# Optimization experiments

Hardware: AMD Instinct MI355X
Metric: run time of the kernel (lower is better)

## Reference

```python
import jax, jax.numpy as jnp
import numpy as np

B1, B2, CHUNK, HID, T = 64, 16, 128, 64, 131072
N_CHUNKS = 128


def setup_inputs() -> dict:
    key = jax.random.key(0)
    ks = jax.random.split(key, 12)
    # positive prices so log(p) is finite
    p = jax.random.uniform(ks[0], (T, 2), jnp.float32) * 2.0 + 0.5
    inds = jax.random.randint(ks[1], (B1,), 0, 100000, dtype=jnp.int32)
    open_slices = jax.random.randint(ks[2], (B1, B2, 1), 0, T, dtype=jnp.int32)
    ls_probs = jax.random.uniform(ks[3], (B1, B2, 1, 1), jnp.float32)
    open_probs = jax.random.uniform(ks[4], (B1, B2, 1, 1), jnp.float32)
    open_hx = jax.random.normal(ks[5], (B1, B2, 2, HID), jnp.float32) * 0.1
    s = 1.0 / np.sqrt(HID)
    # torch nn.LSTM params: gate order i,f,g,o
    W_ih = jax.random.uniform(ks[6], (4 * HID, 2), jnp.float32, -s, s)
    W_hh = jax.random.uniform(ks[7], (4 * HID, HID), jnp.float32, -s, s)
    b_ih = jax.random.uniform(ks[8], (4 * HID,), jnp.float32, -s, s)
    b_hh = jax.random.uniform(ks[9], (4 * HID,), jnp.float32, -s, s)
    W_out = jax.random.uniform(ks[10], (1, HID), jnp.float32, -s, s)
    b_out = jax.random.uniform(ks[11], (1,), jnp.float32, -s, s)
    return {"inds": inds, "p": p, "ls_probs": ls_probs, "open_probs": open_probs,
            "open_slices": open_slices, "open_hx": open_hx,
            "W_ih": W_ih, "W_hh": W_hh, "b_ih": b_ih, "b_hh": b_hh,
            "W_out": W_out, "b_out": b_out, "n_chunks": N_CHUNKS}


def reference(inds, p, ls_probs, open_probs, open_slices, open_hx,
              W_ih, W_hh, b_ih, b_hh, W_out, b_out, n_chunks):
    b1, b2 = open_hx.shape[:2]
    hid = open_hx.shape[-1]
    C = CHUNK
    h0 = open_hx[:, :, 0, :].reshape(b1 * b2, hid)
    c0 = open_hx[:, :, 1, :].reshape(b1 * b2, hid)
    open_logp = jnp.log(p[open_slices])  # (b1, b2, 1, 2)
    # sliding-window gather base: idx[i,j,t] = inds[i] + j + t (per-chunk offset added in scan)
    base = (inds[:, None, None]
            + jnp.arange(b2, dtype=inds.dtype)[None, :, None]
            + jnp.arange(C, dtype=inds.dtype)[None, None, :])  # (b1, b2, C)
    bias = b_ih + b_hh

    def lstm_chunk(x, h, c):  # x: (N, C, 2)
        xg = x @ W_ih.T + bias  # precompute input projection: (N, C, 4H)
        def step(carry, xg_t):
            h, c = carry
            g = xg_t + h @ W_hh.T
            i, f, gg, o = jnp.split(g, 4, axis=-1)
            c = jax.nn.sigmoid(f) * c + jax.nn.sigmoid(i) * jnp.tanh(gg)
            h = jax.nn.sigmoid(o) * jnp.tanh(c)
            return (h, c), h
        (h, c), hs = jax.lax.scan(step, (h, c), xg.swapaxes(0, 1))
        return hs.swapaxes(0, 1), h, c  # (N, C, H)

    def chunk_step(carry, offset):
        h, c, last_nd, loss = carry
        idx = base + offset * C                      # (b1, b2, C)
        p_chunk = p[idx]                             # (b1, b2, C, 2)
        x = p_chunk - p_chunk[:, :, :1, :]           # re-center on first step of chunk
        out, h, c = lstm_chunk(x.reshape(b1 * b2, C, 2), h, c)
        probs = jax.nn.sigmoid(out.reshape(b1, b2, C, hid) @ W_out.T + b_out)  # (b1,b2,C,1)
        not_done = last_nd * jnp.cumprod(1.0 - probs[:, :, :-1], axis=2)       # (b1,b2,C-1,1)
        probs = jnp.concatenate([probs[:, :, :1], probs[:, :, 1:] * not_done], axis=2)
        last_nd = not_done[:, :, -1:, :]
        logp = jnp.log(p_chunk)
        payoff = ls_probs * (logp - open_logp) + (1.0 - ls_probs) * (open_logp - logp)
        loss = loss + jnp.sum(open_probs * probs * payoff)
        return (h, c, last_nd, loss), None

    init = (h0, c0, jnp.ones((b1, b2, 1, 1), p.dtype), jnp.zeros((), p.dtype))
    (_, _, _, loss), _ = jax.lax.scan(chunk_step, init, jnp.arange(n_chunks))
    return loss
```

## Files before the change

### kernel.cpp

```cpp
#include <hip/hip_runtime.h>


#define CH  128
#define HID 64

typedef __fp16 half8 __attribute__((ext_vector_type(8)));
typedef float  f32x4 __attribute__((ext_vector_type(4)));
typedef int    int4v __attribute__((ext_vector_type(4)));

__device__ __forceinline__ float rlf(float v, int l) {
  return __builtin_bit_cast(float, __builtin_amdgcn_readlane(__builtin_bit_cast(int, v), l));
}
__device__ __forceinline__ int packh(float a, float b) {
  return __builtin_bit_cast(int, __builtin_amdgcn_cvt_pkrtz(a, b));
}
__device__ __forceinline__ float frcp(float x) { return __builtin_amdgcn_rcpf(x); }
__device__ __forceinline__ float sigm(float x) { return frcp(1.0f + __expf(-x)); }
__device__ __forceinline__ float tanh_(float x) {
  float e = __expf(2.0f * x);
  return 1.0f - 2.0f * frcp(e + 1.0f);
}
template <int CTRL, int RMASK>
__device__ __forceinline__ float dpp_add(float v) {
  int x = __builtin_amdgcn_update_dpp(0, __builtin_bit_cast(int, v), CTRL, RMASK, 0xF, true);
  return v + __builtin_bit_cast(float, x);
}
__device__ __forceinline__ float dpp_xor1(float v) {
  int x = __builtin_amdgcn_update_dpp(0, __builtin_bit_cast(int, v), 0xB1, 0xF, 0xF, true);
  return __builtin_bit_cast(float, x);
}
__device__ __forceinline__ float dpp_wave_sum(float v) {
  v = dpp_add<0x111, 0xF>(v);
  v = dpp_add<0x112, 0xF>(v);
  v = dpp_add<0x114, 0xF>(v);
  v = dpp_add<0x118, 0xF>(v);
  v = dpp_add<0x142, 0xA>(v);
  v = dpp_add<0x143, 0xC>(v);
  return v;
}

__global__ __attribute__((amdgpu_flat_work_group_size(128, 128), amdgpu_waves_per_eu(2, 2)))
void pc_lstm_kernel(const int* __restrict__ inds,
                    const float* __restrict__ p,
                    const float* __restrict__ ls_probs,
                    const float* __restrict__ open_probs,
                    const int* __restrict__ open_slices,
                    const float* __restrict__ open_hx,
                    const float* __restrict__ W_ih,
                    const float* __restrict__ W_hh,
                    const float* __restrict__ b_ih,
                    const float* __restrict__ b_hh,
                    const float* __restrict__ W_out,
                    const float* __restrict__ b_out,
                    const int* __restrict__ n_chunks_p,
                    float* __restrict__ out)
{
  __shared__ __fp16 ring[2][CH][HID];
  __shared__ int prod;
  __shared__ int cons;

  const int tid  = threadIdx.x;
  const int wv   = tid >> 6;
  const int lane = tid & 63;
  const int s    = blockIdx.x;
  const int n_chunks = n_chunks_p[0];
  const int tbase = inds[s >> 4] + (s & 15);
  const float2* p2 = (const float2*)p;

  if (tid == 0) { prod = 0; cons = 0; }
  __syncthreads();

  if (wv == 0) {
    const int kg = lane >> 4;
    const int cc = lane & 15;

    half8 Wb[32];
#pragma unroll
    for (int t = 0; t < 16; ++t) {
#pragma unroll
      for (int kc = 0; kc < 2; ++kc) {
        const float* wp = W_hh + (16 * t + cc) * HID + 32 * kc + 8 * kg;
        half8 w;
#pragma unroll
        for (int j = 0; j < 8; ++j) w[j] = (__fp16)wp[j];
        Wb[2 * t + kc] = w;
      }
    }

    float wxa[4], wxb[4], bb[4];
#pragma unroll
    for (int g = 0; g < 4; ++g) {
      const int r = g * HID + lane;
      wxa[g] = W_ih[2 * r];
      wxb[g] = W_ih[2 * r + 1];
      bb[g]  = b_ih[r] + b_hh[r];
    }
    float h = open_hx[(s * 2 + 0) * HID + lane];
    float c = open_hx[(s * 2 + 1) * HID + lane];

    int ia0[4], ia1[4];
#pragma unroll
    for (int w = 0; w < 4; ++w) {
      ia0[w] = 4 * (8 * kg + 2 * w);
      ia1[w] = 4 * (32 + 8 * kg + 2 * w);
    }

    const bool u1 = (lane & 16) != 0;
    const bool u2 = (lane & 32) != 0;
    const f32x4 zero4 = {0.f, 0.f, 0.f, 0.f};

    float2 curA = p2[tbase + lane];
    float2 curB = p2[tbase + HID + lane];
    float2 nxtA = curA, nxtB = curB;

    for (int off = 0; off < n_chunks; ++off) {
      if (off) { curA = nxtA; curB = nxtB; }
      const float px0 = rlf(curA.x, 0);
      const float px1 = rlf(curA.y, 0);
      float2 xA, xB;
      xA.x = curA.x - px0; xA.y = curA.y - px1;
      xB.x = curB.x - px0; xB.y = curB.y - px1;
      if (off + 1 < n_chunks) {
        const int nb = tbase + (off + 1) * CH;
        nxtA = p2[nb + lane];
        nxtB = p2[nb + HID + lane];
      }
      while (__hip_atomic_load(&cons, __ATOMIC_ACQUIRE, __HIP_MEMORY_SCOPE_WORKGROUP) + 2 <= off)
        __builtin_amdgcn_s_sleep(8);

      __fp16* slot = &ring[off & 1][0][0];
#pragma unroll
      for (int hf = 0; hf < 2; ++hf) {
        const float xcx = hf ? xB.x : xA.x;
        const float xcy = hf ? xB.y : xA.y;
#pragma unroll 1
        for (int tl = 0; tl < 64; ++tl) {
          const int hp = packh(h, dpp_xor1(h));
          int4v A0, A1;
#pragma unroll
          for (int w = 0; w < 4; ++w) {
            A0[w] = __builtin_amdgcn_ds_bpermute(ia0[w], hp);
            A1[w] = __builtin_amdgcn_ds_bpermute(ia1[w], hp);
          }
          const half8 a0 = __builtin_bit_cast(half8, A0);
          const half8 a1 = __builtin_bit_cast(half8, A1);

          const float x0 = rlf(xcx, tl);
          const float x1 = rlf(xcy, tl);

          float pa[4];
#pragma unroll
          for (int g = 0; g < 4; ++g) {
            f32x4 q0 = __builtin_amdgcn_mfma_f32_16x16x32_f16(a0, Wb[8 * g + 0], zero4, 0, 0, 0);
            q0       = __builtin_amdgcn_mfma_f32_16x16x32_f16(a1, Wb[8 * g + 1], q0,    0, 0, 0);
            f32x4 q1 = __builtin_amdgcn_mfma_f32_16x16x32_f16(a0, Wb[8 * g + 2], zero4, 0, 0, 0);
            q1       = __builtin_amdgcn_mfma_f32_16x16x32_f16(a1, Wb[8 * g + 3], q1,    0, 0, 0);
            f32x4 q2 = __builtin_amdgcn_mfma_f32_16x16x32_f16(a0, Wb[8 * g + 4], zero4, 0, 0, 0);
            q2       = __builtin_amdgcn_mfma_f32_16x16x32_f16(a1, Wb[8 * g + 5], q2,    0, 0, 0);
            f32x4 q3 = __builtin_amdgcn_mfma_f32_16x16x32_f16(a0, Wb[8 * g + 6], zero4, 0, 0, 0);
            q3       = __builtin_amdgcn_mfma_f32_16x16x32_f16(a1, Wb[8 * g + 7], q3,    0, 0, 0);
            const float s01 = u1 ? q1[0] : q0[0];
            const float s23 = u1 ? q3[0] : q2[0];
            const float dg  = u2 ? s23 : s01;
            pa[g] = fmaf(x0, wxa[g], fmaf(x1, wxb[g], dg + bb[g]));
          }

          const float ig = sigm(pa[0]);
          const float fg = sigm(pa[1]);
          const float gg = tanh_(pa[2]);
          const float og = sigm(pa[3]);
          c = fmaf(fg, c, ig * gg);
          h = og * tanh_(c);

          const int tt = hf * 64 + tl;
          slot[tt * HID + lane] = (__fp16)h;
        }
      }
      if (lane == 0)
        __hip_atomic_store(&prod, off + 1, __ATOMIC_RELEASE, __HIP_MEMORY_SCOPE_WORKGROUP);
    }
  } else {
    const float wo   = W_out[lane];
    const float bout = b_out[0];
    const int   os   = open_slices[s];
    const float OL   = __logf(p[2 * os]) + __logf(p[2 * os + 1]);
    const float coef = open_probs[s] * (2.0f * ls_probs[s] - 1.0f);

    float S = 1.0f, D = 1.0f, lsum = 0.0f, psum = 0.0f;

    for (int off = 0; off < n_chunks; ++off) {
      const int cb = tbase + off * CH;
      const float2 cA = p2[cb + lane];
      const float2 cB = p2[cb + HID + lane];
      const float LA = __logf(cA.x) + __logf(cA.y);
      const float LB = __logf(cB.x) + __logf(cB.y);

      while (__hip_atomic_load(&prod, __ATOMIC_ACQUIRE, __HIP_MEMORY_SCOPE_WORKGROUP) <= off)
        __builtin_amdgcn_s_sleep(32);

      const __fp16* slot = &ring[off & 1][0][0];
#pragma unroll 1
      for (int tt = 0; tt < CH; ++tt) {
        const float hv = (float)slot[tt * HID + lane];
        const float z  = rlf(dpp_wave_sum(hv * wo), 63);
        const float pr = sigm(z + bout);
        const float Lt = (tt < 64) ? rlf(LA, tt) : rlf(LB, tt - 64);
        const float pn = (tt == 0) ? pr : pr * D;
        lsum = fmaf(pn, Lt, lsum);
        psum += pn;
        if (tt == 0)           D = S * (1.0f - pr);
        else if (tt < CH - 1)  D *= (1.0f - pr);
        else                   S = D;
      }
      if (lane == 0)
        __hip_atomic_store(&cons, off + 1, __ATOMIC_RELEASE, __HIP_MEMORY_SCOPE_WORKGROUP);
    }
    if (lane == 0) atomicAdd(out, coef * (lsum - OL * psum));
  }
}

extern "C" void kernel_launch(void* const* d_in, const int* in_sizes, int n_in,
                              void* d_out, int out_size, void* d_ws, size_t ws_size,
                              hipStream_t stream) {
  (void)hipMemsetAsync(d_out, 0, sizeof(float), stream);

  pc_lstm_kernel<<<dim3(1024), dim3(128), 0, stream>>>(
      (const int*)d_in[0],
      (const float*)d_in[1],
      (const float*)d_in[2],
      (const float*)d_in[3],
      (const int*)d_in[4],
      (const float*)d_in[5],
      (const float*)d_in[6],
      (const float*)d_in[7],
      (const float*)d_in[8],
      (const float*)d_in[9],
      (const float*)d_in[10],
      (const float*)d_in[11],
      (const int*)d_in[12],
      (float*)d_out);
}
```

Baseline: 7.032 ms.

## Pack four sequences per wave into the MFMA batch and shrink grid

Each block now processes four LSTM sequences instead of one. The 16 batch rows of the 16x16x32 MFMA carry 4 sequences × 4 hidden slices, so the MFMA work that was mostly wasted on a single sequence now serves four, and the grid shrinks from 1024 to 256 blocks. The producer wave also computes the W_out dot product itself through a row-level DPP reduction and passes only per-step logits through LDS, replacing the fp16 hidden-state ring. The cost is four times the gate math per lane per step, fewer blocks to fill the GPU, and a relaxed waves-per-EU hint.

```diff
diff --git a/kernel.cpp b/kernel.cpp
--- a/kernel.cpp
+++ b/kernel.cpp
@@ -8,8 +8,11 @@
 typedef float  f32x4 __attribute__((ext_vector_type(4)));
 typedef int    int4v __attribute__((ext_vector_type(4)));
 
-__device__ __forceinline__ float rlf(float v, int l) {
-  return __builtin_bit_cast(float, __builtin_amdgcn_readlane(__builtin_bit_cast(int, v), l));
+__device__ __forceinline__ int bperm(int byte_idx, int src) {
+  return __builtin_amdgcn_ds_bpermute(byte_idx, src);
+}
+__device__ __forceinline__ float bpermf(int byte_idx, float src) {
+  return __builtin_bit_cast(float, __builtin_amdgcn_ds_bpermute(byte_idx, __builtin_bit_cast(int, src)));
 }
 __device__ __forceinline__ int packh(float a, float b) {
   return __builtin_bit_cast(int, __builtin_amdgcn_cvt_pkrtz(a, b));
@@ -29,17 +32,21 @@
   int x = __builtin_amdgcn_update_dpp(0, __builtin_bit_cast(int, v), 0xB1, 0xF, 0xF, true);
   return __builtin_bit_cast(float, x);
 }
-__device__ __forceinline__ float dpp_wave_sum(float v) {
+__device__ __forceinline__ float dpp_row_sum(float v) {
   v = dpp_add<0x111, 0xF>(v);
   v = dpp_add<0x112, 0xF>(v);
   v = dpp_add<0x114, 0xF>(v);
   v = dpp_add<0x118, 0xF>(v);
+  return v;
+}
+__device__ __forceinline__ float dpp_wave_sum(float v) {
+  v = dpp_row_sum(v);
   v = dpp_add<0x142, 0xA>(v);
   v = dpp_add<0x143, 0xC>(v);
   return v;
 }
 
-__global__ __attribute__((amdgpu_flat_work_group_size(128, 128), amdgpu_waves_per_eu(2, 2)))
+__global__ __attribute__((amdgpu_flat_work_group_size(128, 128), amdgpu_waves_per_eu(1, 2)))
 void pc_lstm_kernel(const int* __restrict__ inds,
                     const float* __restrict__ p,
                     const float* __restrict__ ls_probs,
@@ -55,7 +62,7 @@
                     const int* __restrict__ n_chunks_p,
                     float* __restrict__ out)
 {
-  __shared__ __fp16 ring[2][CH][HID];
+  __shared__ float zring[2][CH][4];
   __shared__ int prod;
   __shared__ int cons;
 
@@ -64,15 +71,18 @@
   const int lane = tid & 63;
   const int s    = blockIdx.x;
   const int n_chunks = n_chunks_p[0];
-  const int tbase = inds[s >> 4] + (s & 15);
+  const int q    = lane >> 4;
+  const int cc   = lane & 15;
+  const int sq   = 4 * s + q;
+  const int tb   = inds[sq >> 4] + (sq & 15);
   const float2* p2 = (const float2*)p;
+  const int xbase = 4 * (16 * q);
 
   if (tid == 0) { prod = 0; cons = 0; }
   __syncthreads();
 
   if (wv == 0) {
     const int kg = lane >> 4;
-    const int cc = lane & 15;
 
     half8 Wb[32];
 #pragma unroll
@@ -87,135 +97,158 @@
       }
     }
 
-    float wxa[4], wxb[4], bb[4];
-#pragma unroll
-    for (int g = 0; g < 4; ++g) {
-      const int r = g * HID + lane;
-      wxa[g] = W_ih[2 * r];
-      wxb[g] = W_ih[2 * r + 1];
-      bb[g]  = b_ih[r] + b_hh[r];
-    }
-    float h = open_hx[(s * 2 + 0) * HID + lane];
-    float c = open_hx[(s * 2 + 1) * HID + lane];
-
-    int ia0[4], ia1[4];
-#pragma unroll
-    for (int w = 0; w < 4; ++w) {
-      ia0[w] = 4 * (8 * kg + 2 * w);
-      ia1[w] = 4 * (32 + 8 * kg + 2 * w);
-    }
-
-    const bool u1 = (lane & 16) != 0;
-    const bool u2 = (lane & 32) != 0;
+    float wxa[4][4], wxb[4][4], bb[4][4];
+#pragma unroll
+    for (int g = 0; g < 4; ++g)
+#pragma unroll
+      for (int u = 0; u < 4; ++u) {
+        const int r = g * HID + cc + 16 * u;
+        wxa[g][u] = W_ih[2 * r];
+        wxb[g][u] = W_ih[2 * r + 1];
+        bb[g][u]  = b_ih[r] + b_hh[r];
+      }
+    float wo[4];
+#pragma unroll
+    for (int u = 0; u < 4; ++u) wo[u] = W_out[cc + 16 * u];
+
+    float h[4], c[4];
+#pragma unroll
+    for (int u = 0; u < 4; ++u) {
+      h[u] = open_hx[(sq * 2 + 0) * HID + cc + 16 * u];
+      c[u] = open_hx[(sq * 2 + 1) * HID + cc + 16 * u];
+    }
+
+    const int qa = cc >> 2;
+    int idxA[4];
+#pragma unroll
+    for (int w = 0; w < 4; ++w)
+      idxA[w] = 4 * (16 * qa + ((8 * kg) & 15) + 2 * w);
+    const bool kgLow = (kg < 2);
     const f32x4 zero4 = {0.f, 0.f, 0.f, 0.f};
 
-    float2 curA = p2[tbase + lane];
-    float2 curB = p2[tbase + HID + lane];
-    float2 nxtA = curA, nxtB = curB;
-
     for (int off = 0; off < n_chunks; ++off) {
-      if (off) { curA = nxtA; curB = nxtB; }
-      const float px0 = rlf(curA.x, 0);
-      const float px1 = rlf(curA.y, 0);
-      float2 xA, xB;
-      xA.x = curA.x - px0; xA.y = curA.y - px1;
-      xB.x = curB.x - px0; xB.y = curB.y - px1;
-      if (off + 1 < n_chunks) {
-        const int nb = tbase + (off + 1) * CH;
-        nxtA = p2[nb + lane];
-        nxtB = p2[nb + HID + lane];
+      float xsx[8], xsy[8];
+      {
+        float2 tmp[8];
+        const long cb = (long)tb + (long)off * CH;
+#pragma unroll
+        for (int m = 0; m < 8; ++m) tmp[m] = p2[cb + cc + 16 * m];
+        const float px0 = bpermf(xbase, tmp[0].x);
+        const float px1 = bpermf(xbase, tmp[0].y);
+#pragma unroll
+        for (int m = 0; m < 8; ++m) {
+          xsx[m] = tmp[m].x - px0;
+          xsy[m] = tmp[m].y - px1;
+        }
       }
       while (__hip_atomic_load(&cons, __ATOMIC_ACQUIRE, __HIP_MEMORY_SCOPE_WORKGROUP) + 2 <= off)
         __builtin_amdgcn_s_sleep(8);
 
-      __fp16* slot = &ring[off & 1][0][0];
-#pragma unroll
-      for (int hf = 0; hf < 2; ++hf) {
-        const float xcx = hf ? xB.x : xA.x;
-        const float xcy = hf ? xB.y : xA.y;
+      float* zslot = &zring[off & 1][0][0];
+#pragma unroll
+      for (int m = 0; m < 8; ++m) {
 #pragma unroll 1
-        for (int tl = 0; tl < 64; ++tl) {
-          const int hp = packh(h, dpp_xor1(h));
+        for (int tt = 0; tt < 16; ++tt) {
+          const int t = 16 * m + tt;
+          const float hx0 = dpp_xor1(h[0]), hx1 = dpp_xor1(h[1]);
+          const float hx2 = dpp_xor1(h[2]), hx3 = dpp_xor1(h[3]);
+          const int hp0 = packh(h[0], hx0), hp1 = packh(h[1], hx1);
+          const int hp2 = packh(h[2], hx2), hp3 = packh(h[3], hx3);
+          const int hA = kgLow ? hp0 : hp1;
+          const int hB = kgLow ? hp2 : hp3;
           int4v A0, A1;
 #pragma unroll
           for (int w = 0; w < 4; ++w) {
-            A0[w] = __builtin_amdgcn_ds_bpermute(ia0[w], hp);
-            A1[w] = __builtin_amdgcn_ds_bpermute(ia1[w], hp);
+            A0[w] = bperm(idxA[w], hA);
+            A1[w] = bperm(idxA[w], hB);
           }
           const half8 a0 = __builtin_bit_cast(half8, A0);
           const half8 a1 = __builtin_bit_cast(half8, A1);
 
-          const float x0 = rlf(xcx, tl);
-          const float x1 = rlf(xcy, tl);
-
-          float pa[4];
-#pragma unroll
-          for (int g = 0; g < 4; ++g) {
-            f32x4 q0 = __builtin_amdgcn_mfma_f32_16x16x32_f16(a0, Wb[8 * g + 0], zero4, 0, 0, 0);
-            q0       = __builtin_amdgcn_mfma_f32_16x16x32_f16(a1, Wb[8 * g + 1], q0,    0, 0, 0);
-            f32x4 q1 = __builtin_amdgcn_mfma_f32_16x16x32_f16(a0, Wb[8 * g + 2], zero4, 0, 0, 0);
-            q1       = __builtin_amdgcn_mfma_f32_16x16x32_f16(a1, Wb[8 * g + 3], q1,    0, 0, 0);
-            f32x4 q2 = __builtin_amdgcn_mfma_f32_16x16x32_f16(a0, Wb[8 * g + 4], zero4, 0, 0, 0);
-            q2       = __builtin_amdgcn_mfma_f32_16x16x32_f16(a1, Wb[8 * g + 5], q2,    0, 0, 0);
-            f32x4 q3 = __builtin_amdgcn_mfma_f32_16x16x32_f16(a0, Wb[8 * g + 6], zero4, 0, 0, 0);
-            q3       = __builtin_amdgcn_mfma_f32_16x16x32_f16(a1, Wb[8 * g + 7], q3,    0, 0, 0);
-            const float s01 = u1 ? q1[0] : q0[0];
-            const float s23 = u1 ? q3[0] : q2[0];
-            const float dg  = u2 ? s23 : s01;
-            pa[g] = fmaf(x0, wxa[g], fmaf(x1, wxb[g], dg + bb[g]));
+          const int xi = xbase + 4 * tt;
+          const float x0 = bpermf(xi, xsx[m]);
+          const float x1 = bpermf(xi, xsy[m]);
+
+#pragma unroll
+          for (int u = 0; u < 4; ++u) {
+            f32x4 e0 = __builtin_amdgcn_mfma_f32_16x16x32_f16(a0, Wb[     2 * u], zero4, 0, 0, 0);
+            e0       = __builtin_amdgcn_mfma_f32_16x16x32_f16(a1, Wb[ 1 + 2 * u], e0,    0, 0, 0);
+            f32x4 e1 = __builtin_amdgcn_mfma_f32_16x16x32_f16(a0, Wb[ 8 + 2 * u], zero4, 0, 0, 0);
+            e1       = __builtin_amdgcn_mfma_f32_16x16x32_f16(a1, Wb[ 9 + 2 * u], e1,    0, 0, 0);
+            f32x4 e2 = __builtin_amdgcn_mfma_f32_16x16x32_f16(a0, Wb[16 + 2 * u], zero4, 0, 0, 0);
+            e2       = __builtin_amdgcn_mfma_f32_16x16x32_f16(a1, Wb[17 + 2 * u], e2,    0, 0, 0);
+            f32x4 e3 = __builtin_amdgcn_mfma_f32_16x16x32_f16(a0, Wb[24 + 2 * u], zero4, 0, 0, 0);
+            e3       = __builtin_amdgcn_mfma_f32_16x16x32_f16(a1, Wb[25 + 2 * u], e3,    0, 0, 0);
+
+            const float pa0 = fmaf(x0, wxa[0][u], fmaf(x1, wxb[0][u], e0[0] + bb[0][u]));
+            const float pa1 = fmaf(x0, wxa[1][u], fmaf(x1, wxb[1][u], e1[0] + bb[1][u]));
+            const float pa2 = fmaf(x0, wxa[2][u], fmaf(x1, wxb[2][u], e2[0] + bb[2][u]));
+            const float pa3 = fmaf(x0, wxa[3][u], fmaf(x1, wxb[3][u], e3[0] + bb[3][u]));
+
+            const float ig = sigm(pa0);
+            const float fg = sigm(pa1);
+            const float gg = tanh_(pa2);
+            const float og = sigm(pa3);
+            c[u] = fmaf(fg, c[u], ig * gg);
+            h[u] = og * tanh_(c[u]);
           }
 
-          const float ig = sigm(pa[0]);
-          const float fg = sigm(pa[1]);
-          const float gg = tanh_(pa[2]);
-          const float og = sigm(pa[3]);
-          c = fmaf(fg, c, ig * gg);
-          h = og * tanh_(c);
-
-          const int tt = hf * 64 + tl;
-          slot[tt * HID + lane] = (__fp16)h;
+          float part = h[0] * wo[0];
+          part = fmaf(h[1], wo[1], part);
+          part = fmaf(h[2], wo[2], part);
+          part = fmaf(h[3], wo[3], part);
+          part = dpp_row_sum(part);
+          if (cc == 15) zslot[t * 4 + q] = part;
         }
       }
       if (lane == 0)
         __hip_atomic_store(&prod, off + 1, __ATOMIC_RELEASE, __HIP_MEMORY_SCOPE_WORKGROUP);
     }
   } else {
-    const float wo   = W_out[lane];
     const float bout = b_out[0];
-    const int   os   = open_slices[s];
+    const int   os   = open_slices[sq];
     const float OL   = __logf(p[2 * os]) + __logf(p[2 * os + 1]);
-    const float coef = open_probs[s] * (2.0f * ls_probs[s] - 1.0f);
+    const float coef = open_probs[sq] * (2.0f * ls_probs[sq] - 1.0f);
 
     float S = 1.0f, D = 1.0f, lsum = 0.0f, psum = 0.0f;
 
     for (int off = 0; off < n_chunks; ++off) {
-      const int cb = tbase + off * CH;
-      const float2 cA = p2[cb + lane];
-      const float2 cB = p2[cb + HID + lane];
-      const float LA = __logf(cA.x) + __logf(cA.y);
-      const float LB = __logf(cB.x) + __logf(cB.y);
-
+      float L[8];
+      {
+        const long cb = (long)tb + (long)off * CH;
+#pragma unroll
+        for (int m = 0; m < 8; ++m) {
+          const float2 t2 = p2[cb + cc + 16 * m];
+          L[m] = __logf(t2.x) + __logf(t2.y);
+        }
+      }
       while (__hip_atomic_load(&prod, __ATOMIC_ACQUIRE, __HIP_MEMORY_SCOPE_WORKGROUP) <= off)
         __builtin_amdgcn_s_sleep(32);
 
-      const __fp16* slot = &ring[off & 1][0][0];
+      const float* zs = &zring[off & 1][0][0];
+#pragma unroll
+      for (int m = 0; m < 8; ++m) {
 #pragma unroll 1
-      for (int tt = 0; tt < CH; ++tt) {
-        const float hv = (float)slot[tt * HID + lane];
-        const float z  = rlf(dpp_wave_sum(hv * wo), 63);
-        const float pr = sigm(z + bout);
-        const float Lt = (tt < 64) ? rlf(LA, tt) : rlf(LB, tt - 64);
-        const float pn = (tt == 0) ? pr : pr * D;
-        lsum = fmaf(pn, Lt, lsum);
-        psum += pn;
-        if (tt == 0)           D = S * (1.0f - pr);
-        else if (tt < CH - 1)  D *= (1.0f - pr);
-        else                   S = D;
+        for (int tt = 0; tt < 16; ++tt) {
+          const int t = 16 * m + tt;
+          const float z  = zs[t * 4 + q];
+          const float pr = sigm(z + bout);
+          const float Lt = bpermf(xbase + 4 * tt, L[m]);
+          const float pn = (t == 0) ? pr : pr * D;
+          lsum = fmaf(pn, Lt, lsum);
+          psum += pn;
+          if (t == 0)           D = S * (1.0f - pr);
+          else if (t < CH - 1)  D *= (1.0f - pr);
+          else                  S = D;
+        }
       }
       if (lane == 0)
         __hip_atomic_store(&cons, off + 1, __ATOMIC_RELEASE, __HIP_MEMORY_SCOPE_WORKGROUP);
     }
-    if (lane == 0) atomicAdd(out, coef * (lsum - OL * psum));
+    float v = coef * (lsum - OL * psum);
+    v = (cc == 0) ? v : 0.0f;
+    v = dpp_wave_sum(v);
+    if (lane == 63) atomicAdd(out, v);
   }
 }
 
@@ -224,7 +257,7 @@
                               hipStream_t stream) {
   (void)hipMemsetAsync(d_out, 0, sizeof(float), stream);
 
-  pc_lstm_kernel<<<dim3(1024), dim3(128), 0, stream>>>(
+  pc_lstm_kernel<<<dim3(256), dim3(128), 0, stream>>>(
       (const int*)d_in[0],
       (const float*)d_in[1],
       (const float*)d_in[2],
```

Result: slower. 10.50 ms (+49.3%).

## Split LSTM gate matvec between MFMA and VALU fdot2 paths

Applied to the files above, without the earlier changes.

The recurrent matvec is split by gate: the i and f gates stay on 16 MFMA instructions (half the previous 32), while the g and o gates are computed on the vector ALU with per-lane packed fp16 dot products (fdot2) over weight rows held in registers, with h broadcast through ds_bpermute. The aim is to shorten the serial per-step MFMA dependency chain by running the matrix and vector units in parallel. In exchange it adds 32 bpermutes and 64 dot2 ops per step and raises register pressure with 64 extra half2 weight registers.

```diff
diff --git a/kernel.cpp b/kernel.cpp
--- a/kernel.cpp
+++ b/kernel.cpp
@@ -5,6 +5,7 @@
 #define HID 64
 
 typedef __fp16 half8 __attribute__((ext_vector_type(8)));
+typedef __fp16 half2v __attribute__((ext_vector_type(2)));
 typedef float  f32x4 __attribute__((ext_vector_type(4)));
 typedef int    int4v __attribute__((ext_vector_type(4)));
 
@@ -74,9 +75,9 @@
     const int kg = lane >> 4;
     const int cc = lane & 15;
 
-    half8 Wb[32];
-#pragma unroll
-    for (int t = 0; t < 16; ++t) {
+    half8 Wb[16];
+#pragma unroll
+    for (int t = 0; t < 8; ++t) {
 #pragma unroll
       for (int kc = 0; kc < 2; ++kc) {
         const float* wp = W_hh + (16 * t + cc) * HID + 32 * kc + 8 * kg;
@@ -84,6 +85,18 @@
 #pragma unroll
         for (int j = 0; j < 8; ++j) w[j] = (__fp16)wp[j];
         Wb[2 * t + kc] = w;
+      }
+    }
+
+    half2v Wg[32], Wo[32];
+    {
+      const float2* rg = (const float2*)(W_hh + (2 * HID + lane) * HID);
+      const float2* ro = (const float2*)(W_hh + (3 * HID + lane) * HID);
+#pragma unroll
+      for (int j = 0; j < 32; ++j) {
+        float2 vg = rg[j], vo = ro[j];
+        Wg[j] = __builtin_bit_cast(half2v, packh(vg.x, vg.y));
+        Wo[j] = __builtin_bit_cast(half2v, packh(vo.x, vo.y));
       }
     }
 
@@ -136,6 +149,7 @@
 #pragma unroll 1
         for (int tl = 0; tl < 64; ++tl) {
           const int hp = packh(h, dpp_xor1(h));
+
           int4v A0, A1;
 #pragma unroll
           for (int w = 0; w < 4; ++w) {
@@ -148,27 +162,52 @@
           const float x0 = rlf(xcx, tl);
           const float x1 = rlf(xcy, tl);
 
-          float pa[4];
-#pragma unroll
-          for (int g = 0; g < 4; ++g) {
-            f32x4 q0 = __builtin_amdgcn_mfma_f32_16x16x32_f16(a0, Wb[8 * g + 0], zero4, 0, 0, 0);
-            q0       = __builtin_amdgcn_mfma_f32_16x16x32_f16(a1, Wb[8 * g + 1], q0,    0, 0, 0);
-            f32x4 q1 = __builtin_amdgcn_mfma_f32_16x16x32_f16(a0, Wb[8 * g + 2], zero4, 0, 0, 0);
-            q1       = __builtin_amdgcn_mfma_f32_16x16x32_f16(a1, Wb[8 * g + 3], q1,    0, 0, 0);
-            f32x4 q2 = __builtin_amdgcn_mfma_f32_16x16x32_f16(a0, Wb[8 * g + 4], zero4, 0, 0, 0);
-            q2       = __builtin_amdgcn_mfma_f32_16x16x32_f16(a1, Wb[8 * g + 5], q2,    0, 0, 0);
-            f32x4 q3 = __builtin_amdgcn_mfma_f32_16x16x32_f16(a0, Wb[8 * g + 6], zero4, 0, 0, 0);
-            q3       = __builtin_amdgcn_mfma_f32_16x16x32_f16(a1, Wb[8 * g + 7], q3,    0, 0, 0);
-            const float s01 = u1 ? q1[0] : q0[0];
-            const float s23 = u1 ? q3[0] : q2[0];
-            const float dg  = u2 ? s23 : s01;
-            pa[g] = fmaf(x0, wxa[g], fmaf(x1, wxb[g], dg + bb[g]));
+          f32x4 q0 = __builtin_amdgcn_mfma_f32_16x16x32_f16(a0, Wb[0],  zero4, 0, 0, 0);
+          q0       = __builtin_amdgcn_mfma_f32_16x16x32_f16(a1, Wb[1],  q0,    0, 0, 0);
+          f32x4 q1 = __builtin_amdgcn_mfma_f32_16x16x32_f16(a0, Wb[2],  zero4, 0, 0, 0);
+          q1       = __builtin_amdgcn_mfma_f32_16x16x32_f16(a1, Wb[3],  q1,    0, 0, 0);
+          f32x4 q2 = __builtin_amdgcn_mfma_f32_16x16x32_f16(a0, Wb[4],  zero4, 0, 0, 0);
+          q2       = __builtin_amdgcn_mfma_f32_16x16x32_f16(a1, Wb[5],  q2,    0, 0, 0);
+          f32x4 q3 = __builtin_amdgcn_mfma_f32_16x16x32_f16(a0, Wb[6],  zero4, 0, 0, 0);
+          q3       = __builtin_amdgcn_mfma_f32_16x16x32_f16(a1, Wb[7],  q3,    0, 0, 0);
+          f32x4 r0 = __builtin_amdgcn_mfma_f32_16x16x32_f16(a0, Wb[8],  zero4, 0, 0, 0);
+          r0       = __builtin_amdgcn_mfma_f32_16x16x32_f16(a1, Wb[9],  r0,    0, 0, 0);
+          f32x4 r1 = __builtin_amdgcn_mfma_f32_16x16x32_f16(a0, Wb[10], zero4, 0, 0, 0);
+          r1       = __builtin_amdgcn_mfma_f32_16x16x32_f16(a1, Wb[11], r1,    0, 0, 0);
+          f32x4 r2 = __builtin_amdgcn_mfma_f32_16x16x32_f16(a0, Wb[12], zero4, 0, 0, 0);
+          r2       = __builtin_amdgcn_mfma_f32_16x16x32_f16(a1, Wb[13], r2,    0, 0, 0);
+          f32x4 r3 = __builtin_amdgcn_mfma_f32_16x16x32_f16(a0, Wb[14], zero4, 0, 0, 0);
+          r3       = __builtin_amdgcn_mfma_f32_16x16x32_f16(a1, Wb[15], r3,    0, 0, 0);
+
+          float gA = fmaf(x0, wxa[2], bb[2]);
+          float gB = x1 * wxb[2];
+          float oA = fmaf(x0, wxa[3], bb[3]);
+          float oB = x1 * wxb[3];
+#pragma unroll
+          for (int j = 0; j < 16; ++j) {
+            const half2v hb0 = __builtin_bit_cast(half2v,
+                __builtin_amdgcn_ds_bpermute(8 * (2 * j), hp));
+            const half2v hb1 = __builtin_bit_cast(half2v,
+                __builtin_amdgcn_ds_bpermute(8 * (2 * j + 1), hp));
+            gA = __builtin_amdgcn_fdot2(hb0, Wg[2 * j],     gA, false);
+            oA = __builtin_amdgcn_fdot2(hb0, Wo[2 * j],     oA, false);
+            gB = __builtin_amdgcn_fdot2(hb1, Wg[2 * j + 1], gB, false);
+            oB = __builtin_amdgcn_fdot2(hb1, Wo[2 * j + 1], oB, false);
           }
 
-          const float ig = sigm(pa[0]);
-          const float fg = sigm(pa[1]);
-          const float gg = tanh_(pa[2]);
-          const float og = sigm(pa[3]);
+          const float si01 = u1 ? q1[0] : q0[0];
+          const float si23 = u1 ? q3[0] : q2[0];
+          const float di   = u2 ? si23 : si01;
+          const float sf01 = u1 ? r1[0] : r0[0];
+          const float sf23 = u1 ? r3[0] : r2[0];
+          const float df   = u2 ? sf23 : sf01;
+          const float pai = fmaf(x0, wxa[0], fmaf(x1, wxb[0], di + bb[0]));
+          const float paf = fmaf(x0, wxa[1], fmaf(x1, wxb[1], df + bb[1]));
+
+          const float ig = sigm(pai);
+          const float fg = sigm(paf);
+          const float gg = tanh_(gA + gB);
+          const float og = sigm(oA + oB);
           c = fmaf(fg, c, ig * gg);
           h = og * tanh_(c);
 
```

Result: slower. 9.394 ms (+33.6%).

## Compute output gate on VALU with packed FMA while MFMA handles other gates

Applied to the files above, without the earlier changes.

The output-gate recurrent projection moves off the matrix cores. Each lane now holds its own fp32 W_hh row and computes the dot product with v_pk_fma_f32, reading h broadcast from a small shared buffer. These VALU FMAs are interleaved between the MFMAs of the remaining three gates, and the gates are reordered (g, i, f) so the activations can overlap with outstanding matrix work. This cuts the MFMA count per step by a quarter, at the cost of more VGPRs for the 64 fp32 weights. It also adds an LDS write and reads per step with no explicit barrier, relying on single-wave execution.

```diff
diff --git a/kernel.cpp b/kernel.cpp
--- a/kernel.cpp
+++ b/kernel.cpp
@@ -6,6 +6,7 @@
 
 typedef __fp16 half8 __attribute__((ext_vector_type(8)));
 typedef float  f32x4 __attribute__((ext_vector_type(4)));
+typedef float  f32x2 __attribute__((ext_vector_type(2)));
 typedef int    int4v __attribute__((ext_vector_type(4)));
 
 __device__ __forceinline__ float rlf(float v, int l) {
@@ -37,6 +38,9 @@
   v = dpp_add<0x142, 0xA>(v);
   v = dpp_add<0x143, 0xC>(v);
   return v;
+}
+__device__ __forceinline__ void pkfma(f32x2& acc, f32x2 a, f32x2 b) {
+  asm("v_pk_fma_f32 %0, %1, %2, %0" : "+v"(acc) : "v"(a), "v"(b));
 }
 
 __global__ __attribute__((amdgpu_flat_work_group_size(128, 128), amdgpu_waves_per_eu(2, 2)))
@@ -56,6 +60,7 @@
                     float* __restrict__ out)
 {
   __shared__ __fp16 ring[2][CH][HID];
+  __shared__ float  hbuf[HID];
   __shared__ int prod;
   __shared__ int cons;
 
@@ -74,17 +79,27 @@
     const int kg = lane >> 4;
     const int cc = lane & 15;
 
-    half8 Wb[32];
-#pragma unroll
-    for (int t = 0; t < 16; ++t) {
-#pragma unroll
-      for (int kc = 0; kc < 2; ++kc) {
-        const float* wp = W_hh + (16 * t + cc) * HID + 32 * kc + 8 * kg;
-        half8 w;
-#pragma unroll
-        for (int j = 0; j < 8; ++j) w[j] = (__fp16)wp[j];
-        Wb[2 * t + kc] = w;
-      }
+    half8 Wb[24];
+#pragma unroll
+    for (int gt = 0; gt < 3; ++gt) {
+#pragma unroll
+      for (int tt = 0; tt < 4; ++tt) {
+#pragma unroll
+        for (int kc = 0; kc < 2; ++kc) {
+          const float* wp = W_hh + (16 * (4 * gt + tt) + cc) * HID + 32 * kc + 8 * kg;
+          half8 w;
+#pragma unroll
+          for (int j = 0; j < 8; ++j) w[j] = (__fp16)wp[j];
+          Wb[8 * gt + 2 * tt + kc] = w;
+        }
+      }
+    }
+
+    f32x2 wo2[32];
+    {
+      const f32x2* wrow = (const f32x2*)(W_hh + (3 * HID + lane) * HID);
+#pragma unroll
+      for (int j = 0; j < 32; ++j) wo2[j] = wrow[j];
     }
 
     float wxa[4], wxb[4], bb[4];
@@ -98,20 +113,23 @@
     float h = open_hx[(s * 2 + 0) * HID + lane];
     float c = open_hx[(s * 2 + 1) * HID + lane];
 
-    int ia0[4], ia1[4];
-#pragma unroll
-    for (int w = 0; w < 4; ++w) {
-      ia0[w] = 4 * (8 * kg + 2 * w);
-      ia1[w] = 4 * (32 + 8 * kg + 2 * w);
-    }
+    int ia[4];
+#pragma unroll
+    for (int w = 0; w < 4; ++w) ia[w] = 4 * (8 * kg + 2 * w);
 
     const bool u1 = (lane & 16) != 0;
     const bool u2 = (lane & 32) != 0;
     const f32x4 zero4 = {0.f, 0.f, 0.f, 0.f};
+    const f32x4* hb4 = (const f32x4*)hbuf;
 
     float2 curA = p2[tbase + lane];
     float2 curB = p2[tbase + HID + lane];
     float2 nxtA = curA, nxtB = curB;
+
+#define OSTEP(J) { \
+    const f32x4 h4 = hb4[J]; \
+    pkfma(oacc0, __builtin_shufflevector(h4, h4, 0, 1), wo2[2 * (J)]); \
+    pkfma(oacc1, __builtin_shufflevector(h4, h4, 2, 3), wo2[2 * (J) + 1]); }
 
     for (int off = 0; off < n_chunks; ++off) {
       if (off) { curA = nxtA; curB = nxtB; }
@@ -135,12 +153,13 @@
         const float xcy = hf ? xB.y : xA.y;
 #pragma unroll 1
         for (int tl = 0; tl < 64; ++tl) {
+          hbuf[lane] = h;
           const int hp = packh(h, dpp_xor1(h));
           int4v A0, A1;
 #pragma unroll
           for (int w = 0; w < 4; ++w) {
-            A0[w] = __builtin_amdgcn_ds_bpermute(ia0[w], hp);
-            A1[w] = __builtin_amdgcn_ds_bpermute(ia1[w], hp);
+            A0[w] = __builtin_amdgcn_ds_bpermute(ia[w], hp);
+            A1[w] = __builtin_amdgcn_ds_bpermute(ia[w] + 128, hp);
           }
           const half8 a0 = __builtin_bit_cast(half8, A0);
           const half8 a1 = __builtin_bit_cast(half8, A1);
@@ -148,27 +167,55 @@
           const float x0 = rlf(xcx, tl);
           const float x1 = rlf(xcy, tl);
 
-          float pa[4];
-#pragma unroll
-          for (int g = 0; g < 4; ++g) {
-            f32x4 q0 = __builtin_amdgcn_mfma_f32_16x16x32_f16(a0, Wb[8 * g + 0], zero4, 0, 0, 0);
-            q0       = __builtin_amdgcn_mfma_f32_16x16x32_f16(a1, Wb[8 * g + 1], q0,    0, 0, 0);
-            f32x4 q1 = __builtin_amdgcn_mfma_f32_16x16x32_f16(a0, Wb[8 * g + 2], zero4, 0, 0, 0);
-            q1       = __builtin_amdgcn_mfma_f32_16x16x32_f16(a1, Wb[8 * g + 3], q1,    0, 0, 0);
-            f32x4 q2 = __builtin_amdgcn_mfma_f32_16x16x32_f16(a0, Wb[8 * g + 4], zero4, 0, 0, 0);
-            q2       = __builtin_amdgcn_mfma_f32_16x16x32_f16(a1, Wb[8 * g + 5], q2,    0, 0, 0);
-            f32x4 q3 = __builtin_amdgcn_mfma_f32_16x16x32_f16(a0, Wb[8 * g + 6], zero4, 0, 0, 0);
-            q3       = __builtin_amdgcn_mfma_f32_16x16x32_f16(a1, Wb[8 * g + 7], q3,    0, 0, 0);
-            const float s01 = u1 ? q1[0] : q0[0];
-            const float s23 = u1 ? q3[0] : q2[0];
-            const float dg  = u2 ? s23 : s01;
-            pa[g] = fmaf(x0, wxa[g], fmaf(x1, wxb[g], dg + bb[g]));
-          }
-
-          const float ig = sigm(pa[0]);
-          const float fg = sigm(pa[1]);
-          const float gg = tanh_(pa[2]);
-          const float og = sigm(pa[3]);
+          f32x2 oacc0, oacc1;
+          oacc0[0] = fmaf(x0, wxa[3], bb[3]);
+          oacc0[1] = x1 * wxb[3];
+          oacc1[0] = 0.0f; oacc1[1] = 0.0f;
+
+          f32x4 s0 = __builtin_amdgcn_mfma_f32_16x16x32_f16(a0, Wb[16], zero4, 0, 0, 0); OSTEP(0);
+          f32x4 s1 = __builtin_amdgcn_mfma_f32_16x16x32_f16(a0, Wb[18], zero4, 0, 0, 0); OSTEP(1);
+          f32x4 s2 = __builtin_amdgcn_mfma_f32_16x16x32_f16(a0, Wb[20], zero4, 0, 0, 0); OSTEP(2);
+          f32x4 s3 = __builtin_amdgcn_mfma_f32_16x16x32_f16(a0, Wb[22], zero4, 0, 0, 0); OSTEP(3);
+          s0 = __builtin_amdgcn_mfma_f32_16x16x32_f16(a1, Wb[17], s0, 0, 0, 0); OSTEP(4);
+          s1 = __builtin_amdgcn_mfma_f32_16x16x32_f16(a1, Wb[19], s1, 0, 0, 0); OSTEP(5);
+          s2 = __builtin_amdgcn_mfma_f32_16x16x32_f16(a1, Wb[21], s2, 0, 0, 0); OSTEP(6);
+          s3 = __builtin_amdgcn_mfma_f32_16x16x32_f16(a1, Wb[23], s3, 0, 0, 0); OSTEP(7);
+          const float sg01 = u1 ? s1[0] : s0[0];
+          const float sg23 = u1 ? s3[0] : s2[0];
+          const float dg   = u2 ? sg23 : sg01;
+          const float pag  = fmaf(x0, wxa[2], fmaf(x1, wxb[2], dg + bb[2]));
+          const float gg   = tanh_(pag);
+
+          f32x4 q0 = __builtin_amdgcn_mfma_f32_16x16x32_f16(a0, Wb[0], zero4, 0, 0, 0); OSTEP(8);
+          f32x4 q1 = __builtin_amdgcn_mfma_f32_16x16x32_f16(a0, Wb[2], zero4, 0, 0, 0); OSTEP(9);
+          f32x4 q2 = __builtin_amdgcn_mfma_f32_16x16x32_f16(a0, Wb[4], zero4, 0, 0, 0); OSTEP(10);
+          f32x4 q3 = __builtin_amdgcn_mfma_f32_16x16x32_f16(a0, Wb[6], zero4, 0, 0, 0); OSTEP(11);
+          q0 = __builtin_amdgcn_mfma_f32_16x16x32_f16(a1, Wb[1], q0, 0, 0, 0); OSTEP(12);
+          q1 = __builtin_amdgcn_mfma_f32_16x16x32_f16(a1, Wb[3], q1, 0, 0, 0); OSTEP(13);
+          q2 = __builtin_amdgcn_mfma_f32_16x16x32_f16(a1, Wb[5], q2, 0, 0, 0); OSTEP(14);
+          q3 = __builtin_amdgcn_mfma_f32_16x16x32_f16(a1, Wb[7], q3, 0, 0, 0); OSTEP(15);
+          const float si01 = u1 ? q1[0] : q0[0];
+          const float si23 = u1 ? q3[0] : q2[0];
+          const float di   = u2 ? si23 : si01;
+          const float pai  = fmaf(x0, wxa[0], fmaf(x1, wxb[0], di + bb[0]));
+          const float ig   = sigm(pai);
+
+          f32x4 r0 = __builtin_amdgcn_mfma_f32_16x16x32_f16(a0, Wb[8],  zero4, 0, 0, 0);
+          f32x4 r1 = __builtin_amdgcn_mfma_f32_16x16x32_f16(a0, Wb[10], zero4, 0, 0, 0);
+          const float osum = (oacc0[0] + oacc0[1]) + (oacc1[0] + oacc1[1]);
+          f32x4 r2 = __builtin_amdgcn_mfma_f32_16x16x32_f16(a0, Wb[12], zero4, 0, 0, 0);
+          const float og = sigm(osum);
+          f32x4 r3 = __builtin_amdgcn_mfma_f32_16x16x32_f16(a0, Wb[14], zero4, 0, 0, 0);
+          r0 = __builtin_amdgcn_mfma_f32_16x16x32_f16(a1, Wb[9],  r0, 0, 0, 0);
+          r1 = __builtin_amdgcn_mfma_f32_16x16x32_f16(a1, Wb[11], r1, 0, 0, 0);
+          r2 = __builtin_amdgcn_mfma_f32_16x16x32_f16(a1, Wb[13], r2, 0, 0, 0);
+          r3 = __builtin_amdgcn_mfma_f32_16x16x32_f16(a1, Wb[15], r3, 0, 0, 0);
+          const float sf01 = u1 ? r1[0] : r0[0];
+          const float sf23 = u1 ? r3[0] : r2[0];
+          const float df   = u2 ? sf23 : sf01;
+          const float paf  = fmaf(x0, wxa[1], fmaf(x1, wxb[1], df + bb[1]));
+          const float fg   = sigm(paf);
+
           c = fmaf(fg, c, ig * gg);
           h = og * tanh_(c);
 
@@ -179,6 +226,7 @@
       if (lane == 0)
         __hip_atomic_store(&prod, off + 1, __ATOMIC_RELEASE, __HIP_MEMORY_SCOPE_WORKGROUP);
     }
+#undef OSTEP
   } else {
     const float wo   = W_out[lane];
     const float bout = b_out[0];
```

Result: slower. 10.16 ms (+44.6%).
